# Kernel optimization log

Measured on AMD Instinct MI355X. Metric: run time of the kernel, lower is better.

Reference implementation:

```python
import jax, jax.numpy as jnp
from jax import lax
import numpy as np

K_F = 3                      # propagation kernel
NUM = K_F * K_F - 1          # 8 non-reference neighbors
IDX_REF = NUM // 2           # 4
PROP_TIME = 18
GAMMA = 0.5                  # affinity_gamma (TGASS)
EPS_AFF = 1e-8


def setup_inputs() -> dict:
    key = jax.random.key(0)
    k1, k2, k3, k4, k5 = jax.random.split(key, 5)
    B, H, W = 4, 352, 1216
    feat_init = jax.random.uniform(k1, (B, 1, H, W), jnp.float32) * 10.0   # initial depth
    guidance = jax.random.normal(k2, (B, NUM, H, W), jnp.float32)
    confidence = jax.random.uniform(k3, (B, 1, H, W), jnp.float32)
    # conv_offset_aff: Conv2d(ch_g=8 -> 3*num=24, k=3, pad=1). Zero-init in the
    # module is a training init; use small random weights for a meaningful test.
    w_oa = jax.random.normal(k4, (3 * NUM, NUM, 3, 3), jnp.float32) * 0.05
    b_oa = jax.random.normal(k5, (3 * NUM,), jnp.float32) * 0.01
    aff_scale = jnp.array([GAMMA * NUM], jnp.float32)  # TGASS learnable scale
    return {"feat_init": feat_init, "guidance": guidance, "confidence": confidence,
            "w_oa": w_oa, "b_oa": b_oa, "aff_scale": aff_scale}


def _offset_affinity(guidance, w_oa, b_oa, aff_scale):
    B, _, H, W = guidance.shape
    oa = lax.conv_general_dilated(guidance, w_oa, (1, 1), "SAME",
                                  dimension_numbers=("NCHW", "OIHW", "NCHW"))
    oa = oa + b_oa[None, :, None, None]
    o1, o2, aff = jnp.split(oa, 3, axis=1)            # each [B, 8, H, W]
    offset = jnp.concatenate([o1, o2], axis=1).reshape(B, NUM, 2, H, W)
    zeros_ref = jnp.zeros((B, 1, 2, H, W), offset.dtype)
    offset = jnp.concatenate([offset[:, :IDX_REF], zeros_ref, offset[:, IDX_REF:]],
                             axis=1).reshape(B, -1, H, W)  # [B, 2*9, H, W]
    # TGASS affinity
    aff = jnp.tanh(aff) / (aff_scale[0] + EPS_AFF)
    aff_abs_sum = jnp.sum(jnp.abs(aff), axis=1, keepdims=True) + 1e-4
    aff_abs_sum = jnp.maximum(aff_abs_sum, 1.0)       # TGASS clamp to >= 1
    aff = aff / aff_abs_sum
    aff_ref = 1.0 - jnp.sum(aff, axis=1, keepdims=True)
    aff = jnp.concatenate([aff[:, :IDX_REF], aff_ref, aff[:, IDX_REF:]], axis=1)
    return offset, aff                                 # [B,18,H,W], [B,9,H,W]


def _bilinear(f, ys, xs):
    # f: [H, W]; ys, xs: [K, H, W] float sample coords. Zero outside bounds (DCNv2).
    H, W = f.shape
    y0 = jnp.floor(ys); x0 = jnp.floor(xs)
    wy1 = ys - y0; wy0 = 1.0 - wy1
    wx1 = xs - x0; wx0 = 1.0 - wx1

    def g(yi, xi):
        valid = (yi >= 0) & (yi <= H - 1) & (xi >= 0) & (xi <= W - 1)
        yc = jnp.clip(yi, 0, H - 1).astype(jnp.int32)
        xc = jnp.clip(xi, 0, W - 1).astype(jnp.int32)
        return jnp.where(valid, f[yc, xc], 0.0)

    return (wy0 * wx0 * g(y0, x0) + wy0 * wx1 * g(y0, x0 + 1)
            + wy1 * wx0 * g(y0 + 1, x0) + wy1 * wx1 * g(y0 + 1, x0 + 1))


def _dcn(feat, offset, aff):
    # Modulated deformable conv with w=ones, b=0, stride=1, pad=1, groups=1.
    # feat [B,1,H,W], offset [B,2*9,H,W] ((dy,dx) pairs), aff [B,9,H,W] modulation.
    B, _, H, W = feat.shape
    KK = K_F * K_F
    off = offset.reshape(B, KK, 2, H, W)
    k = jnp.arange(KK)
    ky = (k // K_F - 1).astype(feat.dtype)            # kernel taps, pad=1
    kx = (k % K_F - 1).astype(feat.dtype)
    yg, xg = jnp.meshgrid(jnp.arange(H, dtype=feat.dtype),
                          jnp.arange(W, dtype=feat.dtype), indexing="ij")
    ys = yg[None, None] + ky[None, :, None, None] + off[:, :, 0]  # [B,9,H,W]
    xs = xg[None, None] + kx[None, :, None, None] + off[:, :, 1]
    sampled = jax.vmap(_bilinear)(feat[:, 0], ys, xs)             # [B,9,H,W]
    return jnp.sum(aff * sampled, axis=1, keepdims=True)          # [B,1,H,W]


def reference(feat_init, guidance, confidence, w_oa, b_oa, aff_scale):
    offset, aff = _offset_affinity(guidance, w_oa, b_oa, aff_scale)

    def step(feat, _):
        feat = _dcn(feat * confidence, offset, aff)
        return feat, None

    feat, _ = lax.scan(step, feat_init, None, length=PROP_TIME)
    return feat
```

## Files before the change

kernel.cpp:

```cpp
#include <hip/hip_runtime.h>

#define BB 4
#define HH 352
#define WW 1216
#define HW (HH * WW)
#define NPIX (BB * HW)
#define TX 4

#define PAD_T 5
#define PAD_L 8
#define HP (HH + 2 * PAD_T)
#define WP (WW + 2 * PAD_L)
#define HWP (HP * WP)

#define TROWS 17
#define TCOLS 76
#define TSIZE (TROWS * TCOLS)


__global__ __launch_bounds__(256) void conv_fused_kernel(
    const float* __restrict__ guid, const float* __restrict__ w,
    const float* __restrict__ bias, const float* __restrict__ scale_p,
    unsigned* __restrict__ tab)
{
    int tid = threadIdx.x;
    int bid = blockIdx.x;
    int xcd = bid & 7;
    int u = bid >> 3;
    int role = u & 1;
    int blk = xcd * 209 + (u >> 1);
    int gg = blk * 256 + tid;
    int row = gg / 304;
    int x0 = (gg % 304) * TX;
    int y = row % HH;
    int b = row / HH;
    const float* gb = guid + (size_t)b * 8 * HW;

    if (role == 0) {
        float acc[16][TX];
#pragma unroll
        for (int o = 0; o < 16; ++o) {
            float bv = bias[o];
#pragma unroll
            for (int tx = 0; tx < TX; ++tx) acc[o][tx] = bv;
        }

#pragma unroll 1
        for (int c = 0; c < 8; ++c) {
            float g[3][6];
#pragma unroll
            for (int r = 0; r < 3; ++r) {
                int yy = y + r - 1;
                bool rv = (yy >= 0) && (yy < HH);
                const float* gr = gb + (size_t)c * HW + (size_t)yy * WW;
                if (rv) {
                    const float4 m = *(const float4*)(gr + x0);
                    g[r][1] = m.x; g[r][2] = m.y; g[r][3] = m.z; g[r][4] = m.w;
                    g[r][0] = (x0 > 0) ? gr[x0 - 1] : 0.f;
                    g[r][5] = (x0 + TX < WW) ? gr[x0 + TX] : 0.f;
                } else {
#pragma unroll
                    for (int i = 0; i < 6; ++i) g[r][i] = 0.f;
                }
            }
#pragma unroll
            for (int r = 0; r < 3; ++r) {
#pragma unroll
                for (int i = 0; i < 3; ++i) {
                    int tap = r * 3 + i;
#pragma unroll
                    for (int o = 0; o < 16; ++o) {
                        float wv = w[o * 72 + c * 9 + tap];
#pragma unroll
                        for (int tx = 0; tx < TX; ++tx)
                            acc[o][tx] = fmaf(wv, g[r][i + tx], acc[o][tx]);
                    }
                }
            }
        }

        int idx0 = row * WW + x0;
#pragma unroll
        for (int tx = 0; tx < TX; ++tx) {
            unsigned cw8[8];
#pragma unroll
            for (int n = 0; n < 8; ++n) {
                int k = (n < 4) ? n : n + 1;
                float ky = (float)(k / 3 - 1), kx = (float)(k % 3 - 1);
                float yr = ky + acc[2 * n][tx];
                float xr = kx + acc[2 * n + 1][tx];
                int yq = (int)lrintf((yr + 4.f) * 8192.f);
                int xq = (int)lrintf((xr + 4.f) * 8192.f);
                yq = min(max(yq, 0), 65535);
                xq = min(max(xq, 0), 65535);
                cw8[n] = (unsigned)yq | ((unsigned)xq << 16);
            }
            unsigned* tp = tab + (size_t)(idx0 + tx) * 12;
            *(uint4*)(tp)     = make_uint4(cw8[0], cw8[1], cw8[2], cw8[3]);
            *(uint4*)(tp + 4) = make_uint4(cw8[4], cw8[5], cw8[6], cw8[7]);
        }
    } else {
        float acc[8][TX];
#pragma unroll
        for (int o = 0; o < 8; ++o) {
            float bv = bias[16 + o];
#pragma unroll
            for (int tx = 0; tx < TX; ++tx) acc[o][tx] = bv;
        }

#pragma unroll 1
        for (int c = 0; c < 8; ++c) {
            float g[3][6];
#pragma unroll
            for (int r = 0; r < 3; ++r) {
                int yy = y + r - 1;
                bool rv = (yy >= 0) && (yy < HH);
                const float* gr = gb + (size_t)c * HW + (size_t)yy * WW;
                if (rv) {
                    const float4 m = *(const float4*)(gr + x0);
                    g[r][1] = m.x; g[r][2] = m.y; g[r][3] = m.z; g[r][4] = m.w;
                    g[r][0] = (x0 > 0) ? gr[x0 - 1] : 0.f;
                    g[r][5] = (x0 + TX < WW) ? gr[x0 + TX] : 0.f;
                } else {
#pragma unroll
                    for (int i = 0; i < 6; ++i) g[r][i] = 0.f;
                }
            }
#pragma unroll
            for (int r = 0; r < 3; ++r) {
#pragma unroll
                for (int i = 0; i < 3; ++i) {
                    int tap = r * 3 + i;
#pragma unroll
                    for (int o = 0; o < 8; ++o) {
                        float wv = w[(16 + o) * 72 + c * 9 + tap];
#pragma unroll
                        for (int tx = 0; tx < TX; ++tx)
                            acc[o][tx] = fmaf(wv, g[r][i + tx], acc[o][tx]);
                    }
                }
            }
        }

        float sc = scale_p[0] + 1e-8f;
        int idx0 = row * WW + x0;
#pragma unroll
        for (int tx = 0; tx < TX; ++tx) {
            float a[8];
            float asum = 1e-4f;
#pragma unroll
            for (int n = 0; n < 8; ++n) {
                a[n] = tanhf(acc[n][tx]) / sc;
                asum += fabsf(a[n]);
            }
            asum = fmaxf(asum, 1.0f);
            unsigned q8[8];
#pragma unroll
            for (int n = 0; n < 8; ++n) {
                a[n] = a[n] / asum;
                int q = (int)lrintf((a[n] + 1.f) * 20000.f);
                q = min(max(q, 0), 65535);
                q8[n] = (unsigned)q;
            }
            unsigned* tp = tab + (size_t)(idx0 + tx) * 12 + 8;
            *(uint4*)(tp) = make_uint4(q8[0] | (q8[1] << 16), q8[2] | (q8[3] << 16),
                                       q8[4] | (q8[5] << 16), q8[6] | (q8[7] << 16));
        }
    }
}

template <bool MULCONF>
__global__ __launch_bounds__(512) void prop_step_kernel(
    const float* __restrict__ fsrc, const unsigned* __restrict__ tab,
    const float* __restrict__ conf, float* __restrict__ dst)
{
    __shared__ float tile[TSIZE];

    int bid = blockIdx.x;
    int xcd = bid & 7;
    int s = bid >> 3;
    int gid = xcd * 418 + s;
    int b = gid / 836;
    int r2 = gid % 836;
    int yband = r2 / 19;
    int xb = r2 % 19;
    int t = threadIdx.x;
    int lx = t & 63, ly = t >> 6;
    int x = xb * 64 + lx;
    int y = yband * 8 + ly;
    int idx = (b * HH + y) * WW + x;

    const unsigned* tp = tab + (size_t)idx * 12;
    uint4 t0 = *(const uint4*)(tp);
    uint4 t1 = *(const uint4*)(tp + 4);
    uint4 t2 = *(const uint4*)(tp + 8);
    float cv = MULCONF ? conf[idx] : 0.f;

    {
        const float* gsrc = fsrc + (size_t)b * HWP
                          + (size_t)(yband * 8 + 1) * WP + (xb * 64 + 4);
        for (int i = t; i < TSIZE; i += 512)
            tile[i] = gsrc[(i / TCOLS) * WP + (i % TCOLS)];
    }

    unsigned cw[8] = {t0.x, t0.y, t0.z, t0.w, t1.x, t1.y, t1.z, t1.w};
    float ak[9];
    ak[0] = fmaf((float)(t2.x & 0xffffu), 5e-5f, -1.f);
    ak[1] = fmaf((float)(t2.x >> 16),     5e-5f, -1.f);
    ak[2] = fmaf((float)(t2.y & 0xffffu), 5e-5f, -1.f);
    ak[3] = fmaf((float)(t2.y >> 16),     5e-5f, -1.f);
    ak[5] = fmaf((float)(t2.z & 0xffffu), 5e-5f, -1.f);
    ak[6] = fmaf((float)(t2.z >> 16),     5e-5f, -1.f);
    ak[7] = fmaf((float)(t2.w & 0xffffu), 5e-5f, -1.f);
    ak[8] = fmaf((float)(t2.w >> 16),     5e-5f, -1.f);
    ak[4] = 1.f - (((ak[0] + ak[1]) + (ak[2] + ak[3]))
                 + ((ak[5] + ak[6]) + (ak[7] + ak[8])));

    __syncthreads();

    float fy = (float)ly;
    float fx = (float)lx;
    float res = ak[4] * tile[(ly + 4) * TCOLS + (lx + 4)];
#pragma unroll
    for (int n = 0; n < 8; ++n) {
        float ys = fmaf((float)(cw[n] & 0xffffu), 1.f / 8192.f, fy);
        float xs = fmaf((float)(cw[n] >> 16),     1.f / 8192.f, fx);
        float y0f = floorf(ys), x0f = floorf(xs);
        float wy1 = ys - y0f, wx1 = xs - x0f;
        float wy0 = 1.f - wy1, wx0 = 1.f - wx1;
        int o = (int)y0f * TCOLS + (int)x0f;
        float v00 = tile[o],         v01 = tile[o + 1];
        float v10 = tile[o + TCOLS], v11 = tile[o + TCOLS + 1];
        float sv = wy0 * (wx0 * v00 + wx1 * v01) + wy1 * (wx0 * v10 + wx1 * v11);
        int k = (n < 4) ? n : n + 1;
        res = fmaf(ak[k], sv, res);
    }
    if (MULCONF) {
        res *= cv;
        dst[(size_t)b * HWP + (y + PAD_T) * WP + (x + PAD_L)] = res;
    } else {
        dst[idx] = res;
    }
}

__global__ __launch_bounds__(256) void zero_kernel(float4* __restrict__ p, int n4)
{
    int i = blockIdx.x * blockDim.x + threadIdx.x;
    if (i < n4) p[i] = make_float4(0.f, 0.f, 0.f, 0.f);
}

__global__ __launch_bounds__(256) void mulpad_kernel(
    const float* __restrict__ a, const float* __restrict__ c, float* __restrict__ o)
{
    int t = threadIdx.x;
    int x = blockIdx.x * 64 + (t & 63);
    int y = blockIdx.y * 4 + (t >> 6);
    int b = blockIdx.z;
    int idx = (b * HH + y) * WW + x;
    o[(size_t)b * HWP + (y + PAD_T) * WP + (x + PAD_L)] = a[idx] * c[idx];
}

extern "C" void kernel_launch(void* const* d_in, const int* in_sizes, int n_in,
                              void* d_out, int out_size, void* d_ws, size_t ws_size,
                              hipStream_t stream)
{
    const float* feat_init  = (const float*)d_in[0];
    const float* guidance   = (const float*)d_in[1];
    const float* confidence = (const float*)d_in[2];
    const float* w_oa       = (const float*)d_in[3];
    const float* b_oa       = (const float*)d_in[4];
    const float* aff_scale  = (const float*)d_in[5];
    float* out = (float*)d_out;

    const size_t N = (size_t)NPIX;
    unsigned* tab = (unsigned*)d_ws;
    float* fc0 = (float*)(tab + 12 * N);
    float* fc1 = fc0 + (size_t)BB * HWP;

    const dim3 mgrid(WW / 64, HH / 4, BB);
    const int n4 = 2 * BB * HWP / 4;
    zero_kernel<<<(n4 + 255) / 256, 256, 0, stream>>>((float4*)fc0, n4);
    mulpad_kernel<<<mgrid, 256, 0, stream>>>(feat_init, confidence, fc0);
    conv_fused_kernel<<<2 * 1672, 256, 0, stream>>>(
        guidance, w_oa, b_oa, aff_scale, tab);

    const int pblocks = (WW / 64) * (HH / 8) * BB;
    float* bufs[2] = {fc0, fc1};
    const int T = 18;
    for (int i = 0; i < T; ++i) {
        const float* src = bufs[i & 1];
        if (i < T - 1) {
            float* dst = bufs[(i + 1) & 1];
            prop_step_kernel<true><<<pblocks, 512, 0, stream>>>(
                src, tab, confidence, dst);
        } else {
            prop_step_kernel<false><<<pblocks, 512, 0, stream>>>(
                src, tab, confidence, out);
        }
    }
}
```

Before: 533.7 us.

## Fuse propagation steps into one persistent cooperative kernel with grid sync

Replaces the 18 per-step kernel launches with a single cooperative kernel. Each block owns a fixed range of tiles and loops over all steps, with a grid-wide barrier between steps. This removes per-launch overhead and inter-kernel gaps, but it caps the block count at occupancy, so each block handles tiles serially. It also adds grid-sync cost and loses the XCD-aware block-to-tile mapping.

```diff
diff --git a/kernel.cpp b/kernel.cpp
--- a/kernel.cpp
+++ b/kernel.cpp
@@ -1,4 +1,5 @@
 #include <hip/hip_runtime.h>
+#include <hip/hip_cooperative_groups.h>
 
 #define BB 4
 #define HH 352
@@ -16,6 +17,7 @@
 #define TROWS 17
 #define TCOLS 76
 #define TSIZE (TROWS * TCOLS)
+#define NTILES 3344
 
 
 __global__ __launch_bounds__(256) void conv_fused_kernel(
@@ -169,77 +171,90 @@
     }
 }
 
-template <bool MULCONF>
-__global__ __launch_bounds__(512) void prop_step_kernel(
-    const float* __restrict__ fsrc, const unsigned* __restrict__ tab,
-    const float* __restrict__ conf, float* __restrict__ dst)
-{
+__global__ __launch_bounds__(512) void prop_coop_kernel(
+    float* __restrict__ fc0, float* __restrict__ fc1,
+    const unsigned* __restrict__ tab, const float* __restrict__ conf,
+    float* __restrict__ out)
+{
+    cooperative_groups::grid_group gg = cooperative_groups::this_grid();
     __shared__ float tile[TSIZE];
 
-    int bid = blockIdx.x;
-    int xcd = bid & 7;
-    int s = bid >> 3;
-    int gid = xcd * 418 + s;
-    int b = gid / 836;
-    int r2 = gid % 836;
-    int yband = r2 / 19;
-    int xb = r2 % 19;
     int t = threadIdx.x;
     int lx = t & 63, ly = t >> 6;
-    int x = xb * 64 + lx;
-    int y = yband * 8 + ly;
-    int idx = (b * HH + y) * WW + x;
-
-    const unsigned* tp = tab + (size_t)idx * 12;
-    uint4 t0 = *(const uint4*)(tp);
-    uint4 t1 = *(const uint4*)(tp + 4);
-    uint4 t2 = *(const uint4*)(tp + 8);
-    float cv = MULCONF ? conf[idx] : 0.f;
-
-    {
-        const float* gsrc = fsrc + (size_t)b * HWP
-                          + (size_t)(yband * 8 + 1) * WP + (xb * 64 + 4);
-        for (int i = t; i < TSIZE; i += 512)
-            tile[i] = gsrc[(i / TCOLS) * WP + (i % TCOLS)];
-    }
-
-    unsigned cw[8] = {t0.x, t0.y, t0.z, t0.w, t1.x, t1.y, t1.z, t1.w};
-    float ak[9];
-    ak[0] = fmaf((float)(t2.x & 0xffffu), 5e-5f, -1.f);
-    ak[1] = fmaf((float)(t2.x >> 16),     5e-5f, -1.f);
-    ak[2] = fmaf((float)(t2.y & 0xffffu), 5e-5f, -1.f);
-    ak[3] = fmaf((float)(t2.y >> 16),     5e-5f, -1.f);
-    ak[5] = fmaf((float)(t2.z & 0xffffu), 5e-5f, -1.f);
-    ak[6] = fmaf((float)(t2.z >> 16),     5e-5f, -1.f);
-    ak[7] = fmaf((float)(t2.w & 0xffffu), 5e-5f, -1.f);
-    ak[8] = fmaf((float)(t2.w >> 16),     5e-5f, -1.f);
-    ak[4] = 1.f - (((ak[0] + ak[1]) + (ak[2] + ak[3]))
-                 + ((ak[5] + ak[6]) + (ak[7] + ak[8])));
-
-    __syncthreads();
-
-    float fy = (float)ly;
-    float fx = (float)lx;
-    float res = ak[4] * tile[(ly + 4) * TCOLS + (lx + 4)];
-#pragma unroll
-    for (int n = 0; n < 8; ++n) {
-        float ys = fmaf((float)(cw[n] & 0xffffu), 1.f / 8192.f, fy);
-        float xs = fmaf((float)(cw[n] >> 16),     1.f / 8192.f, fx);
-        float y0f = floorf(ys), x0f = floorf(xs);
-        float wy1 = ys - y0f, wx1 = xs - x0f;
-        float wy0 = 1.f - wy1, wx0 = 1.f - wx1;
-        int o = (int)y0f * TCOLS + (int)x0f;
-        float v00 = tile[o],         v01 = tile[o + 1];
-        float v10 = tile[o + TCOLS], v11 = tile[o + TCOLS + 1];
-        float sv = wy0 * (wx0 * v00 + wx1 * v01) + wy1 * (wx0 * v10 + wx1 * v11);
-        int k = (n < 4) ? n : n + 1;
-        res = fmaf(ak[k], sv, res);
-    }
-    if (MULCONF) {
-        res *= cv;
-        dst[(size_t)b * HWP + (y + PAD_T) * WP + (x + PAD_L)] = res;
-    } else {
-        dst[idx] = res;
+    int nb = gridDim.x;
+    int bid = blockIdx.x;
+    int tl0 = (int)(((long long)bid * NTILES) / nb);
+    int tl1 = (int)(((long long)(bid + 1) * NTILES) / nb);
+
+    for (int step = 0; step < 18; ++step) {
+        const float* src = (step & 1) ? fc1 : fc0;
+        float* dstp = (step & 1) ? fc0 : fc1;
+        bool last = (step == 17);
+
+        for (int tl = tl0; tl < tl1; ++tl) {
+            int b = tl / 836;
+            int r2 = tl % 836;
+            int yband = r2 / 19;
+            int xb = r2 % 19;
+            int x = xb * 64 + lx;
+            int y = yband * 8 + ly;
+            int idx = (b * HH + y) * WW + x;
+
+            const unsigned* tp = tab + (size_t)idx * 12;
+            uint4 t0 = *(const uint4*)(tp);
+            uint4 t1 = *(const uint4*)(tp + 4);
+            uint4 t2 = *(const uint4*)(tp + 8);
+            float cv = last ? 0.f : conf[idx];
+
+            __syncthreads();
+
+            {
+                const float* gsrc = src + (size_t)b * HWP
+                                  + (size_t)(yband * 8 + 1) * WP + (xb * 64 + 4);
+                for (int i = t; i < TSIZE; i += 512)
+                    tile[i] = gsrc[(i / TCOLS) * WP + (i % TCOLS)];
+            }
+
+            unsigned cw[8] = {t0.x, t0.y, t0.z, t0.w, t1.x, t1.y, t1.z, t1.w};
+            float ak[9];
+            ak[0] = fmaf((float)(t2.x & 0xffffu), 5e-5f, -1.f);
+            ak[1] = fmaf((float)(t2.x >> 16),     5e-5f, -1.f);
+            ak[2] = fmaf((float)(t2.y & 0xffffu), 5e-5f, -1.f);
+            ak[3] = fmaf((float)(t2.y >> 16),     5e-5f, -1.f);
+            ak[5] = fmaf((float)(t2.z & 0xffffu), 5e-5f, -1.f);
+            ak[6] = fmaf((float)(t2.z >> 16),     5e-5f, -1.f);
+            ak[7] = fmaf((float)(t2.w & 0xffffu), 5e-5f, -1.f);
+            ak[8] = fmaf((float)(t2.w >> 16),     5e-5f, -1.f);
+            ak[4] = 1.f - (((ak[0] + ak[1]) + (ak[2] + ak[3]))
+                         + ((ak[5] + ak[6]) + (ak[7] + ak[8])));
+
+            __syncthreads();
+
+            float fy = (float)ly;
+            float fx = (float)lx;
+            float res = ak[4] * tile[(ly + 4) * TCOLS + (lx + 4)];
+#pragma unroll
+            for (int n = 0; n < 8; ++n) {
+                float ys = fmaf((float)(cw[n] & 0xffffu), 1.f / 8192.f, fy);
+                float xs = fmaf((float)(cw[n] >> 16),     1.f / 8192.f, fx);
+                float y0f = floorf(ys), x0f = floorf(xs);
+                float wy1 = ys - y0f, wx1 = xs - x0f;
+                float wy0 = 1.f - wy1, wx0 = 1.f - wx1;
+                int o = (int)y0f * TCOLS + (int)x0f;
+                float v00 = tile[o],         v01 = tile[o + 1];
+                float v10 = tile[o + TCOLS], v11 = tile[o + TCOLS + 1];
+                float sv = wy0 * (wx0 * v00 + wx1 * v01)
+                         + wy1 * (wx0 * v10 + wx1 * v11);
+                int k = (n < 4) ? n : n + 1;
+                res = fmaf(ak[k], sv, res);
+            }
+            if (last) {
+                out[idx] = res;
+            } else {
+                dstp[(size_t)b * HWP + (y + PAD_T) * WP + (x + PAD_L)] = res * cv;
+            }
+        }
+        gg.sync();
     }
 }
 
@@ -277,6 +292,19 @@
     float* fc0 = (float*)(tab + 12 * N);
     float* fc1 = fc0 + (size_t)BB * HWP;
 
+    static int coop_blocks = -1;
+    if (coop_blocks < 0) {
+        int maxb = 0, ncu = 0;
+        hipDeviceProp_t prop;
+        if (hipGetDeviceProperties(&prop, 0) == hipSuccess) ncu = prop.multiProcessorCount;
+        if (ncu <= 0) ncu = 256;
+        if (hipOccupancyMaxActiveBlocksPerMultiprocessor(
+                &maxb, prop_coop_kernel, 512, 0) != hipSuccess || maxb < 1)
+            maxb = 1;
+        long long cap = (long long)maxb * ncu;
+        coop_blocks = (int)((cap < NTILES) ? cap : NTILES);
+    }
+
     const dim3 mgrid(WW / 64, HH / 4, BB);
     const int n4 = 2 * BB * HWP / 4;
     zero_kernel<<<(n4 + 255) / 256, 256, 0, stream>>>((float4*)fc0, n4);
@@ -284,18 +312,8 @@
     conv_fused_kernel<<<2 * 1672, 256, 0, stream>>>(
         guidance, w_oa, b_oa, aff_scale, tab);
 
-    const int pblocks = (WW / 64) * (HH / 8) * BB;
-    float* bufs[2] = {fc0, fc1};
-    const int T = 18;
-    for (int i = 0; i < T; ++i) {
-        const float* src = bufs[i & 1];
-        if (i < T - 1) {
-            float* dst = bufs[(i + 1) & 1];
-            prop_step_kernel<true><<<pblocks, 512, 0, stream>>>(
-                src, tab, confidence, dst);
-        } else {
-            prop_step_kernel<false><<<pblocks, 512, 0, stream>>>(
-                src, tab, confidence, out);
-        }
-    }
-}
+    void* args[] = {(void*)&fc0, (void*)&fc1, (void*)&tab,
+                    (void*)&confidence, (void*)&out};
+    hipLaunchCooperativeKernel((void*)prop_coop_kernel, dim3(coop_blocks),
+                               dim3(512), args, 0, stream);
+}
```

Result: slower. 1.718 ms (+221.8%).

## Process two tiles per block and prefetch the second tile during the first

Applied to the files above, without the earlier changes.

Each propagation block now handles two adjacent 64x8 tiles instead of one, and the grid is halved. The second tile's table entries, confidence value and feature halo are loaded from global memory into registers before the first tile is computed, then written to a second shared buffer once the first tile is done. The aim is to hide global load latency behind bilinear-sampling work and to cut per-block launch and setup overhead. The cost is more registers per thread, twice the shared memory per block and fewer blocks in flight, which may lower occupancy.

```diff
diff --git a/kernel.cpp b/kernel.cpp
--- a/kernel.cpp
+++ b/kernel.cpp
@@ -16,6 +16,7 @@
 #define TROWS 17
 #define TCOLS 76
 #define TSIZE (TROWS * TCOLS)
+#define NTILES 3344
 
 
 __global__ __launch_bounds__(256) void conv_fused_kernel(
@@ -174,72 +175,142 @@
     const float* __restrict__ fsrc, const unsigned* __restrict__ tab,
     const float* __restrict__ conf, float* __restrict__ dst)
 {
-    __shared__ float tile[TSIZE];
+    __shared__ float tileA[TSIZE];
+    __shared__ float tileB[TSIZE];
 
     int bid = blockIdx.x;
     int xcd = bid & 7;
     int s = bid >> 3;
-    int gid = xcd * 418 + s;
-    int b = gid / 836;
-    int r2 = gid % 836;
-    int yband = r2 / 19;
-    int xb = r2 % 19;
+    int gidA = xcd * 418 + 2 * s;
+    int gidB = gidA + 1;
     int t = threadIdx.x;
     int lx = t & 63, ly = t >> 6;
-    int x = xb * 64 + lx;
-    int y = yband * 8 + ly;
-    int idx = (b * HH + y) * WW + x;
-
-    const unsigned* tp = tab + (size_t)idx * 12;
-    uint4 t0 = *(const uint4*)(tp);
-    uint4 t1 = *(const uint4*)(tp + 4);
-    uint4 t2 = *(const uint4*)(tp + 8);
-    float cv = MULCONF ? conf[idx] : 0.f;
-
-    {
-        const float* gsrc = fsrc + (size_t)b * HWP
-                          + (size_t)(yband * 8 + 1) * WP + (xb * 64 + 4);
-        for (int i = t; i < TSIZE; i += 512)
-            tile[i] = gsrc[(i / TCOLS) * WP + (i % TCOLS)];
-    }
-
-    unsigned cw[8] = {t0.x, t0.y, t0.z, t0.w, t1.x, t1.y, t1.z, t1.w};
-    float ak[9];
-    ak[0] = fmaf((float)(t2.x & 0xffffu), 5e-5f, -1.f);
-    ak[1] = fmaf((float)(t2.x >> 16),     5e-5f, -1.f);
-    ak[2] = fmaf((float)(t2.y & 0xffffu), 5e-5f, -1.f);
-    ak[3] = fmaf((float)(t2.y >> 16),     5e-5f, -1.f);
-    ak[5] = fmaf((float)(t2.z & 0xffffu), 5e-5f, -1.f);
-    ak[6] = fmaf((float)(t2.z >> 16),     5e-5f, -1.f);
-    ak[7] = fmaf((float)(t2.w & 0xffffu), 5e-5f, -1.f);
-    ak[8] = fmaf((float)(t2.w >> 16),     5e-5f, -1.f);
-    ak[4] = 1.f - (((ak[0] + ak[1]) + (ak[2] + ak[3]))
-                 + ((ak[5] + ak[6]) + (ak[7] + ak[8])));
-
-    __syncthreads();
+
+    int bA = gidA / 836, r2A = gidA % 836;
+    int ybA = r2A / 19, xbA = r2A % 19;
+    int xA = xbA * 64 + lx, yA = ybA * 8 + ly;
+    int idxA = (bA * HH + yA) * WW + xA;
+
+    int bB = gidB / 836, r2B = gidB % 836;
+    int ybB = r2B / 19, xbB = r2B % 19;
+    int xB = xbB * 64 + lx, yB = ybB * 8 + ly;
+    int idxB = (bB * HH + yB) * WW + xB;
+
+    const unsigned* tpA = tab + (size_t)idxA * 12;
+    uint4 a0 = *(const uint4*)(tpA);
+    uint4 a1 = *(const uint4*)(tpA + 4);
+    uint4 a2 = *(const uint4*)(tpA + 8);
+    float cvA = MULCONF ? conf[idxA] : 0.f;
+
+    const float* gsA = fsrc + (size_t)bA * HWP
+                     + (size_t)(ybA * 8 + 1) * WP + (xbA * 64 + 4);
+    float rA0 = gsA[(t / TCOLS) * WP + (t % TCOLS)];
+    float rA1 = gsA[((t + 512) / TCOLS) * WP + ((t + 512) % TCOLS)];
+    float rA2 = (t + 1024 < TSIZE)
+              ? gsA[((t + 1024) / TCOLS) * WP + ((t + 1024) % TCOLS)] : 0.f;
+
+    tileA[t] = rA0;
+    tileA[t + 512] = rA1;
+    if (t + 1024 < TSIZE) tileA[t + 1024] = rA2;
+
+    const unsigned* tpB = tab + (size_t)idxB * 12;
+    uint4 b0 = *(const uint4*)(tpB);
+    uint4 b1 = *(const uint4*)(tpB + 4);
+    uint4 b2 = *(const uint4*)(tpB + 8);
+    float cvB = MULCONF ? conf[idxB] : 0.f;
+
+    const float* gsB = fsrc + (size_t)bB * HWP
+                     + (size_t)(ybB * 8 + 1) * WP + (xbB * 64 + 4);
+    float rB0 = gsB[(t / TCOLS) * WP + (t % TCOLS)];
+    float rB1 = gsB[((t + 512) / TCOLS) * WP + ((t + 512) % TCOLS)];
+    float rB2 = (t + 1024 < TSIZE)
+              ? gsB[((t + 1024) / TCOLS) * WP + ((t + 1024) % TCOLS)] : 0.f;
+
+    asm volatile("s_waitcnt lgkmcnt(0)" ::: "memory");
+    __builtin_amdgcn_s_barrier();
+    __builtin_amdgcn_sched_barrier(0);
 
     float fy = (float)ly;
     float fx = (float)lx;
-    float res = ak[4] * tile[(ly + 4) * TCOLS + (lx + 4)];
-#pragma unroll
-    for (int n = 0; n < 8; ++n) {
-        float ys = fmaf((float)(cw[n] & 0xffffu), 1.f / 8192.f, fy);
-        float xs = fmaf((float)(cw[n] >> 16),     1.f / 8192.f, fx);
-        float y0f = floorf(ys), x0f = floorf(xs);
-        float wy1 = ys - y0f, wx1 = xs - x0f;
-        float wy0 = 1.f - wy1, wx0 = 1.f - wx1;
-        int o = (int)y0f * TCOLS + (int)x0f;
-        float v00 = tile[o],         v01 = tile[o + 1];
-        float v10 = tile[o + TCOLS], v11 = tile[o + TCOLS + 1];
-        float sv = wy0 * (wx0 * v00 + wx1 * v01) + wy1 * (wx0 * v10 + wx1 * v11);
-        int k = (n < 4) ? n : n + 1;
-        res = fmaf(ak[k], sv, res);
+
+    {
+        unsigned cw[8] = {a0.x, a0.y, a0.z, a0.w, a1.x, a1.y, a1.z, a1.w};
+        float ak[9];
+        ak[0] = fmaf((float)(a2.x & 0xffffu), 5e-5f, -1.f);
+        ak[1] = fmaf((float)(a2.x >> 16),     5e-5f, -1.f);
+        ak[2] = fmaf((float)(a2.y & 0xffffu), 5e-5f, -1.f);
+        ak[3] = fmaf((float)(a2.y >> 16),     5e-5f, -1.f);
+        ak[5] = fmaf((float)(a2.z & 0xffffu), 5e-5f, -1.f);
+        ak[6] = fmaf((float)(a2.z >> 16),     5e-5f, -1.f);
+        ak[7] = fmaf((float)(a2.w & 0xffffu), 5e-5f, -1.f);
+        ak[8] = fmaf((float)(a2.w >> 16),     5e-5f, -1.f);
+        ak[4] = 1.f - (((ak[0] + ak[1]) + (ak[2] + ak[3]))
+                     + ((ak[5] + ak[6]) + (ak[7] + ak[8])));
+
+        float res = ak[4] * tileA[(ly + 4) * TCOLS + (lx + 4)];
+#pragma unroll
+        for (int n = 0; n < 8; ++n) {
+            float ys = fmaf((float)(cw[n] & 0xffffu), 1.f / 8192.f, fy);
+            float xs = fmaf((float)(cw[n] >> 16),     1.f / 8192.f, fx);
+            float y0f = floorf(ys), x0f = floorf(xs);
+            float wy1 = ys - y0f, wx1 = xs - x0f;
+            float wy0 = 1.f - wy1, wx0 = 1.f - wx1;
+            int o = (int)y0f * TCOLS + (int)x0f;
+            float v00 = tileA[o],         v01 = tileA[o + 1];
+            float v10 = tileA[o + TCOLS], v11 = tileA[o + TCOLS + 1];
+            float sv = wy0 * (wx0 * v00 + wx1 * v01)
+                     + wy1 * (wx0 * v10 + wx1 * v11);
+            int k = (n < 4) ? n : n + 1;
+            res = fmaf(ak[k], sv, res);
+        }
+        if (MULCONF)
+            dst[(size_t)bA * HWP + (yA + PAD_T) * WP + (xA + PAD_L)] = res * cvA;
+        else
+            dst[idxA] = res;
     }
-    if (MULCONF) {
-        res *= cv;
-        dst[(size_t)b * HWP + (y + PAD_T) * WP + (x + PAD_L)] = res;
-    } else {
-        dst[idx] = res;
+
+    tileB[t] = rB0;
+    tileB[t + 512] = rB1;
+    if (t + 1024 < TSIZE) tileB[t + 1024] = rB2;
+
+    asm volatile("s_waitcnt lgkmcnt(0)" ::: "memory");
+    __builtin_amdgcn_s_barrier();
+    __builtin_amdgcn_sched_barrier(0);
+
+    {
+        unsigned cw[8] = {b0.x, b0.y, b0.z, b0.w, b1.x, b1.y, b1.z, b1.w};
+        float ak[9];
+        ak[0] = fmaf((float)(b2.x & 0xffffu), 5e-5f, -1.f);
+        ak[1] = fmaf((float)(b2.x >> 16),     5e-5f, -1.f);
+        ak[2] = fmaf((float)(b2.y & 0xffffu), 5e-5f, -1.f);
+        ak[3] = fmaf((float)(b2.y >> 16),     5e-5f, -1.f);
+        ak[5] = fmaf((float)(b2.z & 0xffffu), 5e-5f, -1.f);
+        ak[6] = fmaf((float)(b2.z >> 16),     5e-5f, -1.f);
+        ak[7] = fmaf((float)(b2.w & 0xffffu), 5e-5f, -1.f);
+        ak[8] = fmaf((float)(b2.w >> 16),     5e-5f, -1.f);
+        ak[4] = 1.f - (((ak[0] + ak[1]) + (ak[2] + ak[3]))
+                     + ((ak[5] + ak[6]) + (ak[7] + ak[8])));
+
+        float res = ak[4] * tileB[(ly + 4) * TCOLS + (lx + 4)];
+#pragma unroll
+        for (int n = 0; n < 8; ++n) {
+            float ys = fmaf((float)(cw[n] & 0xffffu), 1.f / 8192.f, fy);
+            float xs = fmaf((float)(cw[n] >> 16),     1.f / 8192.f, fx);
+            float y0f = floorf(ys), x0f = floorf(xs);
+            float wy1 = ys - y0f, wx1 = xs - x0f;
+            float wy0 = 1.f - wy1, wx0 = 1.f - wx1;
+            int o = (int)y0f * TCOLS + (int)x0f;
+            float v00 = tileB[o],         v01 = tileB[o + 1];
+            float v10 = tileB[o + TCOLS], v11 = tileB[o + TCOLS + 1];
+            float sv = wy0 * (wx0 * v00 + wx1 * v01)
+                     + wy1 * (wx0 * v10 + wx1 * v11);
+            int k = (n < 4) ? n : n + 1;
+            res = fmaf(ak[k], sv, res);
+        }
+        if (MULCONF)
+            dst[(size_t)bB * HWP + (yB + PAD_T) * WP + (xB + PAD_L)] = res * cvB;
+        else
+            dst[idxB] = res;
     }
 }
 
@@ -284,7 +355,7 @@
     conv_fused_kernel<<<2 * 1672, 256, 0, stream>>>(
         guidance, w_oa, b_oa, aff_scale, tab);
 
-    const int pblocks = (WW / 64) * (HH / 8) * BB;
+    const int pblocks = 1672;
     float* bufs[2] = {fc0, fc1};
     const int T = 18;
     for (int i = 0; i < T; ++i) {
```

Result: faster. 516.1 us (-3.3%).

## Fuse two propagation steps per kernel launch using halo recompute in shared memory

Applied to the files above, without the earlier changes.

Each launch now performs two deformable propagation steps. The first step is computed on an enlarged halo tile held in LDS, and the second reads from that intermediate tile, so 9 launches replace 18. This halves global reads and writes of the feature map and the launch count. In exchange it recomputes the halo region (about 2.7x the pixels in the first stage) and issues extra table and confidence loads for the halo pixels. The padding is widened to cover the larger offset reach.

```diff
diff --git a/kernel.cpp b/kernel.cpp
--- a/kernel.cpp
+++ b/kernel.cpp
@@ -7,15 +7,19 @@
 #define NPIX (BB * HW)
 #define TX 4
 
-#define PAD_T 5
+#define PAD_T 9
 #define PAD_L 8
-#define HP (HH + 2 * PAD_T)
-#define WP (WW + 2 * PAD_L)
+#define HP (HH + 2 * 9)
+#define WP (WW + 8 + 12)
 #define HWP (HP * WP)
 
-#define TROWS 17
-#define TCOLS 76
-#define TSIZE (TROWS * TCOLS)
+#define SROWS 25
+#define SCOLS 84
+#define SSIZE (SROWS * SCOLS)
+#define IROWS 17
+#define ICOLS 76
+#define ISIZE (IROWS * ICOLS)
+#define NTILES 3344
 
 
 __global__ __launch_bounds__(256) void conv_fused_kernel(
@@ -169,40 +173,10 @@
     }
 }
 
-template <bool MULCONF>
-__global__ __launch_bounds__(512) void prop_step_kernel(
-    const float* __restrict__ fsrc, const unsigned* __restrict__ tab,
-    const float* __restrict__ conf, float* __restrict__ dst)
-{
-    __shared__ float tile[TSIZE];
-
-    int bid = blockIdx.x;
-    int xcd = bid & 7;
-    int s = bid >> 3;
-    int gid = xcd * 418 + s;
-    int b = gid / 836;
-    int r2 = gid % 836;
-    int yband = r2 / 19;
-    int xb = r2 % 19;
-    int t = threadIdx.x;
-    int lx = t & 63, ly = t >> 6;
-    int x = xb * 64 + lx;
-    int y = yband * 8 + ly;
-    int idx = (b * HH + y) * WW + x;
-
-    const unsigned* tp = tab + (size_t)idx * 12;
-    uint4 t0 = *(const uint4*)(tp);
-    uint4 t1 = *(const uint4*)(tp + 4);
-    uint4 t2 = *(const uint4*)(tp + 8);
-    float cv = MULCONF ? conf[idx] : 0.f;
-
-    {
-        const float* gsrc = fsrc + (size_t)b * HWP
-                          + (size_t)(yband * 8 + 1) * WP + (xb * 64 + 4);
-        for (int i = t; i < TSIZE; i += 512)
-            tile[i] = gsrc[(i / TCOLS) * WP + (i % TCOLS)];
-    }
-
+template <int STRIDE>
+__device__ __forceinline__ float dcn_px(const float* __restrict__ T,
+    float fy, float fx, uint4 t0, uint4 t1, uint4 t2)
+{
     unsigned cw[8] = {t0.x, t0.y, t0.z, t0.w, t1.x, t1.y, t1.z, t1.w};
     float ak[9];
     ak[0] = fmaf((float)(t2.x & 0xffffu), 5e-5f, -1.f);
@@ -216,11 +190,7 @@
     ak[4] = 1.f - (((ak[0] + ak[1]) + (ak[2] + ak[3]))
                  + ((ak[5] + ak[6]) + (ak[7] + ak[8])));
 
-    __syncthreads();
-
-    float fy = (float)ly;
-    float fx = (float)lx;
-    float res = ak[4] * tile[(ly + 4) * TCOLS + (lx + 4)];
+    float res = ak[4] * T[((int)fy + 4) * STRIDE + (int)fx + 4];
 #pragma unroll
     for (int n = 0; n < 8; ++n) {
         float ys = fmaf((float)(cw[n] & 0xffffu), 1.f / 8192.f, fy);
@@ -228,18 +198,116 @@
         float y0f = floorf(ys), x0f = floorf(xs);
         float wy1 = ys - y0f, wx1 = xs - x0f;
         float wy0 = 1.f - wy1, wx0 = 1.f - wx1;
-        int o = (int)y0f * TCOLS + (int)x0f;
-        float v00 = tile[o],         v01 = tile[o + 1];
-        float v10 = tile[o + TCOLS], v11 = tile[o + TCOLS + 1];
+        int o = (int)y0f * STRIDE + (int)x0f;
+        float v00 = T[o],          v01 = T[o + 1];
+        float v10 = T[o + STRIDE], v11 = T[o + STRIDE + 1];
         float sv = wy0 * (wx0 * v00 + wx1 * v01) + wy1 * (wx0 * v10 + wx1 * v11);
         int k = (n < 4) ? n : n + 1;
         res = fmaf(ak[k], sv, res);
     }
-    if (MULCONF) {
-        res *= cv;
-        dst[(size_t)b * HWP + (y + PAD_T) * WP + (x + PAD_L)] = res;
+    return res;
+}
+
+template <bool LAST>
+__global__ __launch_bounds__(512) void prop_pair_kernel(
+    const float* __restrict__ fsrc, const unsigned* __restrict__ tab,
+    const float* __restrict__ conf, float* __restrict__ dst)
+{
+    __shared__ float S[SSIZE];
+    __shared__ float I[ISIZE];
+
+    int bid = blockIdx.x;
+    int gid = (bid & 7) * 418 + (bid >> 3);
+    int b = gid / 836;
+    int r2 = gid % 836;
+    int yband = r2 / 19;
+    int xb = r2 % 19;
+    int y0 = yband * 8, x0 = xb * 64;
+    int t = threadIdx.x;
+    int lx = t & 63, ly = t >> 6;
+
+    const float* gs = fsrc + (size_t)b * HWP + (size_t)(y0 + 1) * WP + x0;
+    float s0 = gs[(t) / SCOLS * WP + (t) % SCOLS];
+    float s1 = gs[(t + 512) / SCOLS * WP + (t + 512) % SCOLS];
+    float s2 = gs[(t + 1024) / SCOLS * WP + (t + 1024) % SCOLS];
+    float s3 = gs[(t + 1536) / SCOLS * WP + (t + 1536) % SCOLS];
+    float s4 = (t + 2048 < SSIZE)
+             ? gs[(t + 2048) / SCOLS * WP + (t + 2048) % SCOLS] : 0.f;
+
+    auto tload = [&](int p, uint4& c0, uint4& c1, uint4& c2, float& cf,
+                     bool& valid, int& pr, int& pc) {
+        pr = p / ICOLS; pc = p % ICOLS;
+        int yi = y0 - 4 + pr, xi = x0 - 4 + pc;
+        valid = (p < ISIZE) && (yi >= 0) && (yi < HH) && (xi >= 0) && (xi < WW);
+        if (valid) {
+            int idx = (b * HH + yi) * WW + xi;
+            const unsigned* tp = tab + (size_t)idx * 12;
+            c0 = *(const uint4*)(tp);
+            c1 = *(const uint4*)(tp + 4);
+            c2 = *(const uint4*)(tp + 8);
+            cf = conf[idx];
+        } else {
+            c0 = c1 = c2 = make_uint4(0u, 0u, 0u, 0u);
+            cf = 0.f;
+        }
+    };
+
+    uint4 c00, c01, c02, c10, c11, c12;
+    float cf0, cf1;
+    bool v0, v1;
+    int pr0, pc0, pr1, pc1;
+    tload(t, c00, c01, c02, cf0, v0, pr0, pc0);
+    tload(t + 512, c10, c11, c12, cf1, v1, pr1, pc1);
+
+    S[t] = s0;
+    S[t + 512] = s1;
+    S[t + 1024] = s2;
+    S[t + 1536] = s3;
+    if (t + 2048 < SSIZE) S[t + 2048] = s4;
+
+    uint4 c20, c21, c22;
+    float cf2;
+    bool v2;
+    int pr2, pc2;
+    tload(t + 1024, c20, c21, c22, cf2, v2, pr2, pc2);
+
+    int yF = y0 + ly, xF = x0 + lx;
+    int idxF = (b * HH + yF) * WW + xF;
+    const unsigned* tpF = tab + (size_t)idxF * 12;
+    uint4 f0 = *(const uint4*)(tpF);
+    uint4 f1 = *(const uint4*)(tpF + 4);
+    uint4 f2 = *(const uint4*)(tpF + 8);
+    float cvF = LAST ? 0.f : conf[idxF];
+
+    asm volatile("s_waitcnt lgkmcnt(0)" ::: "memory");
+    __builtin_amdgcn_s_barrier();
+    __builtin_amdgcn_sched_barrier(0);
+
+    {
+        float vI = 0.f;
+        if (v0) vI = cf0 * dcn_px<SCOLS>(S, (float)pr0, (float)pc0, c00, c01, c02);
+        I[t] = vI;
+    }
+    {
+        float vI = 0.f;
+        if (v1) vI = cf1 * dcn_px<SCOLS>(S, (float)pr1, (float)pc1, c10, c11, c12);
+        I[t + 512] = vI;
+    }
+    if (t + 1024 < ISIZE) {
+        float vI = 0.f;
+        if (v2) vI = cf2 * dcn_px<SCOLS>(S, (float)pr2, (float)pc2, c20, c21, c22);
+        I[t + 1024] = vI;
+    }
+
+    asm volatile("s_waitcnt lgkmcnt(0)" ::: "memory");
+    __builtin_amdgcn_s_barrier();
+    __builtin_amdgcn_sched_barrier(0);
+
+    float res = dcn_px<ICOLS>(I, (float)ly, (float)lx, f0, f1, f2);
+    if (LAST) {
+        dst[idxF] = res;
     } else {
-        dst[idx] = res;
+        dst[(size_t)b * HWP + (yF + PAD_T) * WP + (xF + PAD_L)] = res * cvF;
     }
 }
 
@@ -284,17 +352,15 @@
     conv_fused_kernel<<<2 * 1672, 256, 0, stream>>>(
         guidance, w_oa, b_oa, aff_scale, tab);
 
-    const int pblocks = (WW / 64) * (HH / 8) * BB;
     float* bufs[2] = {fc0, fc1};
-    const int T = 18;
-    for (int i = 0; i < T; ++i) {
-        const float* src = bufs[i & 1];
-        if (i < T - 1) {
-            float* dst = bufs[(i + 1) & 1];
-            prop_step_kernel<true><<<pblocks, 512, 0, stream>>>(
+    for (int p = 0; p < 9; ++p) {
+        const float* src = bufs[p & 1];
+        if (p < 8) {
+            float* dst = bufs[(p + 1) & 1];
+            prop_pair_kernel<false><<<NTILES, 512, 0, stream>>>(
                 src, tab, confidence, dst);
         } else {
-            prop_step_kernel<false><<<pblocks, 512, 0, stream>>>(
+            prop_pair_kernel<true><<<NTILES, 512, 0, stream>>>(
                 src, tab, confidence, out);
         }
     }
```

After: 559.6 us. +4.8%, slower.
